# Kernel optimization log

Measured on AMD Instinct MI355X. Metric: run time of the kernel, lower is better.

Reference implementation:

```python
import jax, jax.numpy as jnp
import numpy as np

BQ = 64  # query block size
BK = 64  # key block size
PV_SCALE = 1e-3  # pvthreshd (~0..50) -> prob threshold, mirrors int8 P-quantization cutoff


def setup_inputs() -> dict:
    key = jax.random.key(0)
    ks = jax.random.split(key, 6)
    B, H, L, D = 2, 16, 2048, 64
    q = jax.random.normal(ks[0], (B, H, L, D), jnp.float32)
    k = jax.random.normal(ks[1], (B, H, L, D), jnp.float32)
    v = jax.random.normal(ks[2], (B, H, L, D), jnp.float32)
    # per-head tuned thresholds (init defaults / autotune ranges)
    cdfthreshd = 0.85 + 0.14 * jax.random.uniform(ks[3], (H,), jnp.float32)
    simthreshd1 = jax.random.uniform(ks[4], (H,), jnp.float32, minval=-0.3, maxval=0.5)
    pvthreshd = jax.random.uniform(ks[5], (H,), jnp.float32, minval=15.0, maxval=25.0)
    return dict(q=q, k=k, v=v, cdfthreshd=cdfthreshd,
                simthreshd1=simthreshd1, pvthreshd=pvthreshd)


def _sparse_meansim_attention(q, k, v, cdfthreshd, simthreshd1, pvthreshd):
    B, H, L, D = q.shape
    nqb, nkb = L // BQ, L // BK
    scale = 1.0 / jnp.sqrt(jnp.float32(D))

    # smooth_k: subtract per-(B,H) key mean along sequence
    k = k - k.mean(axis=2, keepdims=True)

    qb = q.reshape(B, H, nqb, BQ, D)
    kb = k.reshape(B, H, nkb, BK, D)
    qm = qb.mean(axis=3)  # [B,H,nqb,D]
    km = kb.mean(axis=3)  # [B,H,nkb,D]

    # mean cosine similarity of queries to their block mean -> pooled (prunable) blocks
    qn = jnp.linalg.norm(qb, axis=-1)            # [B,H,nqb,BQ]
    qmn = jnp.linalg.norm(qm, axis=-1)           # [B,H,nqb]
    cos = jnp.einsum('bhnqd,bhnd->bhnq', qb, qm) / (qn * qmn[..., None] + 1e-6)
    pooled = cos.mean(axis=-1) > simthreshd1[None, :, None]  # [B,H,nqb]

    # block-level score map from pooled means, CDF-based top-mass block selection
    s = jnp.einsum('bhid,bhjd->bhij', qm, km) * scale        # [B,H,nqb,nkb]
    p = jax.nn.softmax(s, axis=-1)
    order = jnp.argsort(-p, axis=-1)
    p_sorted = jnp.take_along_axis(p, order, axis=-1)
    excl_cdf = jnp.cumsum(p_sorted, axis=-1) - p_sorted      # exclusive CDF
    keep_sorted = excl_cdf < cdfthreshd[None, :, None, None]
    keep = jnp.take_along_axis(keep_sorted, jnp.argsort(order, axis=-1), axis=-1)

    sink = (jnp.arange(nkb) == 0)  # attention_sink: always keep first key block
    block_mask = keep | (~pooled)[..., None] | sink          # [B,H,nqb,nkb]

    # full attention restricted to selected blocks
    S = jnp.einsum('bhqd,bhkd->bhqk', q, k) * scale          # [B,H,L,L]
    m = jnp.repeat(jnp.repeat(block_mask, BQ, axis=2), BK, axis=3)
    P = jax.nn.softmax(jnp.where(m, S, -jnp.inf), axis=-1)

    # second-stage PV pruning: skip PV accumulation for negligible prob blocks
    Pb = P.reshape(B, H, nqb, BQ, nkb, BK)
    pv_keep = Pb.max(axis=(3, 5)) >= pvthreshd[None, :, None, None] * PV_SCALE
    pv_keep = pv_keep | sink
    Pb = Pb * pv_keep[:, :, :, None, :, None].astype(P.dtype)

    o = jnp.einsum('bhqk,bhkd->bhqd', Pb.reshape(B, H, L, L), v)
    return o


def reference(q, k, v, cdfthreshd, simthreshd1, pvthreshd):
    return _sparse_meansim_attention(q, k, v, cdfthreshd, simthreshd1, pvthreshd)
```

## Files before the change

### kernel.cpp

```cpp
#include <hip/hip_runtime.h>
#include <hip/hip_bf16.h>
#include <math.h>
#include <stdint.h>

#define B 2
#define H 16
#define L 2048
#define D 64
#define NB 32
#define PTS 72

typedef unsigned short u16;
typedef unsigned int u32;
typedef __attribute__((ext_vector_type(2))) unsigned int u32x2;
typedef __attribute__((ext_vector_type(4))) unsigned int u32x4;
typedef __attribute__((ext_vector_type(8))) short s16x8;
typedef __attribute__((ext_vector_type(4))) float f32x4;

union FragU { s16x8 v; u32 u[4]; };

__device__ __forceinline__ u32 pkbf(float a, float b) {
  __hip_bfloat162 h = __float22bfloat162_rn(make_float2(a, b));
  union { __hip_bfloat162 h; u32 u; } cv; cv.h = h; return cv.u;
}
__device__ __forceinline__ float bf2f(u32 u16bits) {
  union { u32 u; float f; } c; c.u = u16bits << 16; return c.f;
}
__device__ __forceinline__ void split4(float4 p, u32x2& hi, u32x2& lo) {
  u32 h01 = pkbf(p.x, p.y), h23 = pkbf(p.z, p.w);
  float rx = p.x - bf2f(h01 & 0xffffu);
  float ry = p.y - bf2f(h01 >> 16);
  float rz = p.z - bf2f(h23 & 0xffffu);
  float rw = p.w - bf2f(h23 >> 16);
  hi = (u32x2){h01, h23};
  lo = (u32x2){pkbf(rx, ry), pkbf(rz, rw)};
}

__global__ __launch_bounds__(256) void k_prep(const float* __restrict__ k,
                                              const float* __restrict__ v,
                                              float* __restrict__ ksum,
                                              u16* __restrict__ khi_g,
                                              u16* __restrict__ klo_g,
                                              u16* __restrict__ vthi_g,
                                              u16* __restrict__ vtlo_g,
                                              float* __restrict__ kbmax) {
  int blk = blockIdx.x, bh = blk >> 5, j = blk & 31, t = threadIdx.x;
  int lane = t & 63, w = t >> 6;
  __shared__ float vt[64 * 65];
  __shared__ float pk_[4][64];
  __shared__ unsigned bmaxS;
  if (t == 0) bmaxS = 0u;
  size_t base = (size_t)blk * 4096;

  int r0 = t >> 3;
  int c8 = (t & 7) * 8;
  float cs[8] = {0.f, 0.f, 0.f, 0.f, 0.f, 0.f, 0.f, 0.f};
  float rmax = 0.f;
#pragma unroll
  for (int it = 0; it < 2; ++it) {
    int r = r0 + 32 * it;
    const float* kp = k + base + r * 64 + c8;
    float4 f0 = *(const float4*)kp;
    float4 f1 = *(const float4*)(kp + 4);
    u32x2 h0, l0, h1, l1;
    split4(f0, h0, l0); split4(f1, h1, l1);
    *(u32x4*)(khi_g + base + r * 64 + c8) = (u32x4){h0[0], h0[1], h1[0], h1[1]};
    *(u32x4*)(klo_g + base + r * 64 + c8) = (u32x4){l0[0], l0[1], l1[0], l1[1]};
    cs[0] += f0.x; cs[1] += f0.y; cs[2] += f0.z; cs[3] += f0.w;
    cs[4] += f1.x; cs[5] += f1.y; cs[6] += f1.z; cs[7] += f1.w;
    float ssq = f0.x*f0.x + f0.y*f0.y + f0.z*f0.z + f0.w*f0.w
              + f1.x*f1.x + f1.y*f1.y + f1.z*f1.z + f1.w*f1.w;
    ssq += __shfl_xor(ssq, 1); ssq += __shfl_xor(ssq, 2); ssq += __shfl_xor(ssq, 4);
    if ((t & 7) == 0) rmax = fmaxf(rmax, ssq);
    const float* vp = v + base + r * 64 + c8;
    float4 g0 = *(const float4*)vp;
    float4 g1 = *(const float4*)(vp + 4);
    vt[(c8 + 0) * 65 + r] = g0.x;
    vt[(c8 + 1) * 65 + r] = g0.y;
    vt[(c8 + 2) * 65 + r] = g0.z;
    vt[(c8 + 3) * 65 + r] = g0.w;
    vt[(c8 + 4) * 65 + r] = g1.x;
    vt[(c8 + 5) * 65 + r] = g1.y;
    vt[(c8 + 6) * 65 + r] = g1.z;
    vt[(c8 + 7) * 65 + r] = g1.w;
  }
  if ((t & 7) == 0) atomicMax(&bmaxS, __float_as_uint(rmax));
#pragma unroll
  for (int i = 0; i < 8; ++i) {
    cs[i] += __shfl_xor(cs[i], 8);
    cs[i] += __shfl_xor(cs[i], 16);
    cs[i] += __shfl_xor(cs[i], 32);
  }
  if (lane < 8) {
    *(float4*)&pk_[w][lane * 8]     = (float4){cs[0], cs[1], cs[2], cs[3]};
    *(float4*)&pk_[w][lane * 8 + 4] = (float4){cs[4], cs[5], cs[6], cs[7]};
  }
  __syncthreads();
  if (t < 64) ksum[(size_t)blk * 64 + t] = pk_[0][t] + pk_[1][t] + pk_[2][t] + pk_[3][t];
  if (t == 0) kbmax[blk] = __uint_as_float(bmaxS);
#pragma unroll
  for (int it = 0; it < 2; ++it) {
    int idx = t + 256 * it, d = idx >> 3, s8 = (idx & 7) * 8;
    const float* vr = &vt[d * 65 + s8];
    float4 f0 = {vr[0], vr[1], vr[2], vr[3]};
    float4 f1 = {vr[4], vr[5], vr[6], vr[7]};
    u32x2 h0, l0, h1, l1;
    split4(f0, h0, l0); split4(f1, h1, l1);
    size_t o = (size_t)bh * 131072 + (size_t)d * 2048 + j * 64 + s8;
    *(u32x4*)(vthi_g + o) = (u32x4){h0[0], h0[1], h1[0], h1[1]};
    *(u32x4*)(vtlo_g + o) = (u32x4){l0[0], l0[1], l1[0], l1[1]};
  }
}

#define RBM_OFF 36864
#define MS_OFF 53760
#define LINV_OFF 54272
#define LPART_OFF 54784
#define QM_OFF 56832
#define FLG_OFF 57344

__global__ __launch_bounds__(256, 2) void k_attn(
    const float* __restrict__ q,
    const float* __restrict__ ksum,
    const u16* __restrict__ khi_g, const u16* __restrict__ klo_g,
    const u16* __restrict__ vthi_g, const u16* __restrict__ vtlo_g,
    const float* __restrict__ cdfthreshd, const float* __restrict__ simthreshd1,
    const float* __restrict__ pvthreshd, const float* __restrict__ kbmax,
    float* __restrict__ out) {
  int blk0 = blockIdx.x;
  int blk = (blk0 & 7) * 64 + (blk0 >> 3);
  int bh = blk >> 4, ip = blk & 15, h = bh & (H - 1);
  int t = threadIdx.x, lane = t & 63, w = t >> 6;
  int m16 = lane & 15, quad = lane >> 4;

  __shared__ __align__(16) uint8_t smem[57376];
  u16*   pbase = (u16*)smem;
  u32*   rbm0  = (u32*)(smem + RBM_OFF);
  float* MS    = (float*)(smem + MS_OFF);
  float* linvS = (float*)(smem + LINV_OFF);
  float* lpart = (float*)(smem + LPART_OFF);
  float* qmS   = (float*)(smem + QM_OFF);
  int*   flg   = (int*)(smem + FLG_OFF);
#define PHQ(qb) (pbase + (qb) * 9216)
#define PLQ(qb) (pbase + 4608 + (qb) * 9216)

  const float* qg0 = q + ((size_t)bh * L + (size_t)(2 * ip) * 64) * D;
  const float* qg1 = qg0 + 64 * D;
  const u16* kh = khi_g + (size_t)bh * (L * D);
  const u16* kl = klo_g + (size_t)bh * (L * D);
  const u16* vh = vthi_g + (size_t)bh * (L * D);
  const u16* vl = vtlo_g + (size_t)bh * (L * D);

  s16x8 qhf[2][4][2], qlf[2][4][2];
#pragma unroll
  for (int qb = 0; qb < 2; ++qb) {
    const float* qgq = qb ? qg1 : qg0;
#pragma unroll
    for (int nt = 0; nt < 4; ++nt)
#pragma unroll
      for (int ks = 0; ks < 2; ++ks) {
        const float* p0 = qgq + (16 * nt + m16) * 64 + ks * 32 + quad * 8;
        float4 a = *(const float4*)p0;
        float4 b2 = *(const float4*)(p0 + 4);
        u32x2 ha, la, hb, lb;
        split4(a, ha, la); split4(b2, hb, lb);
        FragU fh, fl;
        fh.u[0] = ha[0]; fh.u[1] = ha[1]; fh.u[2] = hb[0]; fh.u[3] = hb[1];
        fl.u[0] = la[0]; fl.u[1] = la[1]; fl.u[2] = lb[0]; fl.u[3] = lb[1];
        qhf[qb][nt][ks] = fh.v; qlf[qb][nt][ks] = fl.v;
      }
  }
  for (int e = t; e < 2 * 64 * 33; e += 256)
    rbm0[e] = 0x7F800000u;

  if (w == 0 || w == 2) {
    int qb = w >> 1;
    const float* qgq = qb ? qg1 : qg0;
    float s = 0.f;
    for (int r = 0; r < 64; ++r) s += qgq[r * 64 + lane];
    qmS[qb * 64 + lane] = s * (1.f / 64.f);
  }
  if (w == 1) {
    float m = (lane < 32) ? kbmax[bh * 32 + lane] : 0.f;
    for (int off = 16; off; off >>= 1) m = fmaxf(m, __shfl_xor(m, off, 32));
    if (lane == 0) ((float*)flg)[6] = m;
  }
  __syncthreads();

  bool keepj = false;
  if ((w == 0 || w == 2) && lane < 32) {
    int qb = w >> 1, j = lane;
    const float* qmv = qmS + qb * 64;
    const float* ksp = ksum + (size_t)bh * NB * 64 + j * 64;
    float sv = 0.f;
    for (int d = 0; d < 64; ++d) sv += qmv[d] * ksp[d];
    sv *= (1.f / 64.f) * 0.125f;
    float mx = sv;
    for (int off = 16; off; off >>= 1) mx = fmaxf(mx, __shfl_xor(mx, off, 32));
    float p = expf(sv - mx);
    float sum = p;
    for (int off = 16; off; off >>= 1) sum += __shfl_xor(sum, off, 32);
    p /= sum;
    float excl = 0.f;
    for (int u = 0; u < 32; ++u) {
      float pu = __shfl(p, u, 32);
      if ((pu > p) || (pu == p && u < j)) excl += pu;
    }
    keepj = excl < cdfthreshd[h];
  }
  if (w == 1 || w == 3) {
    int qb = w >> 1, r = lane;
    const float* qgq = qb ? qg1 : qg0;
    const float* qmv = qmS + qb * 64;
    float kmax2 = ((float*)flg)[6];
    float dot = 0.f, qn2 = 0.f, qmn2 = 0.f;
    for (int d = 0; d < 64; ++d) {
      float a = qgq[r * 64 + d], b2 = qmv[d];
      dot += a * b2; qn2 += a * a; qmn2 += b2 * b2;
    }
    float cs = dot / (sqrtf(qn2) * sqrtf(qmn2) + 1e-6f);
    float su = cs;
    for (int off = 32; off; off >>= 1) su += __shfl_xor(su, off);
    if (lane == 0) flg[qb] = (su * (1.f / 64.f)) > simthreshd1[h];
    MS[qb * 64 + r] = sqrtf(qn2 * kmax2) * 0.125f;
  }
  __syncthreads();
  if ((w == 0 || w == 2) && lane < 32) {
    int qb = w >> 1;
    bool bit = keepj || !flg[qb] || (lane == 0);
    unsigned long long bal = __ballot(bit);
    if (lane == 0) flg[2 + qb] = (int)(u32)bal;
  }
  __syncthreads();
  u32 mw0 = (u32)flg[2], mw1 = (u32)flg[3];

  float Mq[2][4];
#pragma unroll
  for (int qb = 0; qb < 2; ++qb)
#pragma unroll
    for (int nt = 0; nt < 4; ++nt) Mq[qb][nt] = MS[qb * 64 + 16 * nt + m16];

  float lp[2][4] = {{0.f,0.f,0.f,0.f},{0.f,0.f,0.f,0.f}};
  {
    u32 mwU = mw0 | mw1;
    int j = (int)__builtin_ctz(mwU);
    u32 rm_ = mwU & (mwU - 1);
    s16x8 ka[2][2], kan[2][2];
    {
      const u16* kr0 = kh + (size_t)(j * 64 + 16 * w + m16) * 64 + quad * 8;
      const u16* kl0 = kl + (size_t)(j * 64 + 16 * w + m16) * 64 + quad * 8;
#pragma unroll
      for (int ks = 0; ks < 2; ++ks) {
        ka[ks][0] = *(const s16x8*)(kr0 + ks * 32);
        ka[ks][1] = *(const s16x8*)(kl0 + ks * 32);
      }
    }
    for (;;) {
      int nj = -1;
      if (rm_) {
        nj = (int)__builtin_ctz(rm_); rm_ &= rm_ - 1;
        const u16* nr = kh + (size_t)(nj * 64 + 16 * w + m16) * 64 + quad * 8;
        const u16* nl = kl + (size_t)(nj * 64 + 16 * w + m16) * 64 + quad * 8;
#pragma unroll
        for (int ks = 0; ks < 2; ++ks) {
          kan[ks][0] = *(const s16x8*)(nr + ks * 32);
          kan[ks][1] = *(const s16x8*)(nl + ks * 32);
        }
      }
#pragma unroll
      for (int qb = 0; qb < 2; ++qb) {
        u32 mm = qb ? mw1 : mw0;
        if (!((mm >> j) & 1u)) continue;
        f32x4 acc[4];
#pragma unroll
        for (int nt = 0; nt < 4; ++nt) acc[nt] = (f32x4){0.f, 0.f, 0.f, 0.f};
#pragma unroll
        for (int ks = 0; ks < 2; ++ks)
#pragma unroll
          for (int nt = 0; nt < 4; ++nt) {
            acc[nt] = __builtin_amdgcn_mfma_f32_16x16x32_bf16(ka[ks][0], qhf[qb][nt][ks], acc[nt], 0, 0, 0);
            acc[nt] = __builtin_amdgcn_mfma_f32_16x16x32_bf16(ka[ks][1], qhf[qb][nt][ks], acc[nt], 0, 0, 0);
            acc[nt] = __builtin_amdgcn_mfma_f32_16x16x32_bf16(ka[ks][0], qlf[qb][nt][ks], acc[nt], 0, 0, 0);
          }
#pragma unroll
        for (int nt = 0; nt < 4; ++nt) {
          float vmax = -1e30f;
#pragma unroll
          for (int reg = 0; reg < 4; ++reg) {
            float s = acc[nt][reg] * 0.125f - Mq[qb][nt];
            lp[qb][nt] += __expf(s);
            vmax = fmaxf(vmax, s);
          }
          vmax = fmaxf(vmax, __shfl_xor(vmax, 16));
          vmax = fmaxf(vmax, __shfl_xor(vmax, 32));
          if (quad == 0)
            atomicMin(rbm0 + qb * (64 * 33) + (16 * nt + m16) * 33 + j,
                      __float_as_uint(fmaxf(-vmax, 0.f)));
        }
      }
      if (nj < 0) break;
#pragma unroll
      for (int ks = 0; ks < 2; ++ks) { ka[ks][0] = kan[ks][0]; ka[ks][1] = kan[ks][1]; }
      j = nj;
    }
  }
#pragma unroll
  for (int qb = 0; qb < 2; ++qb)
#pragma unroll
    for (int nt = 0; nt < 4; ++nt) {
      float s = lp[qb][nt];
      s += __shfl_xor(s, 16); s += __shfl_xor(s, 32);
      if (quad == 0) lpart[w * 128 + qb * 64 + 16 * nt + m16] = s;
    }
  __syncthreads();
  if (t < 128) linvS[t] = 1.f / (lpart[t] + lpart[128 + t] + lpart[256 + t] + lpart[384 + t]);
  __syncthreads();

  if (w < 2 && lane < 32) {
    u32 mm = w ? mw1 : mw0;
    bool keep = (mm >> lane) & 1u;
    if (keep && lane != 0) {
      float thr = pvthreshd[h] * 1e-3f;
      const float* lin = linvS + w * 64;
      const u32* rb = rbm0 + w * (64 * 33);
      float mp = 0.f;
      for (int r = 0; r < 64; ++r) {
        float key = __uint_as_float(rb[r * 33 + lane]);
        mp = fmaxf(mp, __expf(-key) * lin[r]);
      }
      keep = mp >= thr;
    }
    unsigned long long bal = __ballot(keep);
    if (lane == 0) flg[4 + w] = (int)(u32)bal;
  }
  __syncthreads();
  u32 gm0 = (u32)flg[4], gm1 = (u32)flg[5];

  float linq[2][4];
#pragma unroll
  for (int qb = 0; qb < 2; ++qb)
#pragma unroll
    for (int nt = 0; nt < 4; ++nt) linq[qb][nt] = linvS[qb * 64 + 16 * nt + m16];
  f32x4 oacc[2][4];
#pragma unroll
  for (int qb = 0; qb < 2; ++qb)
#pragma unroll
    for (int nt = 0; nt < 4; ++nt) oacc[qb][nt] = (f32x4){0.f, 0.f, 0.f, 0.f};

  {
    u32 gmU = gm0 | gm1;
    int j = -1;
    u32 g2 = gmU;
    s16x8 ka[2][2];
    if (g2) {
      j = (int)__builtin_ctz(g2); g2 &= g2 - 1;
      const u16* kr0 = kh + (size_t)(j * 64 + 16 * w + m16) * 64 + quad * 8;
      const u16* kl0 = kl + (size_t)(j * 64 + 16 * w + m16) * 64 + quad * 8;
#pragma unroll
      for (int ks = 0; ks < 2; ++ks) {
        ka[ks][0] = *(const s16x8*)(kr0 + ks * 32);
        ka[ks][1] = *(const s16x8*)(kl0 + ks * 32);
      }
    }
    while (j >= 0) {
      int in0 = (gm0 >> j) & 1, in1 = (gm1 >> j) & 1;
      s16x8 va[2][2];
      {
        const u16* vr0 = vh + (size_t)(16 * w + m16) * L + j * 64 + quad * 8;
        const u16* vl0 = vl + (size_t)(16 * w + m16) * L + j * 64 + quad * 8;
#pragma unroll
        for (int ks = 0; ks < 2; ++ks) {
          va[ks][0] = *(const s16x8*)(vr0 + ks * 32);
          va[ks][1] = *(const s16x8*)(vl0 + ks * 32);
        }
      }
      f32x4 acc[4];
      if (in0) {
#pragma unroll
        for (int nt = 0; nt < 4; ++nt) acc[nt] = (f32x4){0.f, 0.f, 0.f, 0.f};
#pragma unroll
        for (int ks = 0; ks < 2; ++ks)
#pragma unroll
          for (int nt = 0; nt < 4; ++nt) {
            acc[nt] = __builtin_amdgcn_mfma_f32_16x16x32_bf16(ka[ks][0], qhf[0][nt][ks], acc[nt], 0, 0, 0);
            acc[nt] = __builtin_amdgcn_mfma_f32_16x16x32_bf16(ka[ks][1], qhf[0][nt][ks], acc[nt], 0, 0, 0);
            acc[nt] = __builtin_amdgcn_mfma_f32_16x16x32_bf16(ka[ks][0], qlf[0][nt][ks], acc[nt], 0, 0, 0);
          }
      }
      __syncthreads();
      if (in0) {
#pragma unroll
        for (int nt = 0; nt < 4; ++nt) {
          float4 pv;
          pv.x = __expf(acc[nt][0] * 0.125f - Mq[0][nt]) * linq[0][nt];
          pv.y = __expf(acc[nt][1] * 0.125f - Mq[0][nt]) * linq[0][nt];
          pv.z = __expf(acc[nt][2] * 0.125f - Mq[0][nt]) * linq[0][nt];
          pv.w = __expf(acc[nt][3] * 0.125f - Mq[0][nt]) * linq[0][nt];
          u32x2 hi, lo; split4(pv, hi, lo);
          int off = (16 * nt + m16) * PTS + 16 * w + 4 * quad;
          *(u32x2*)(PHQ(0) + off) = hi;
          *(u32x2*)(PLQ(0) + off) = lo;
        }
      }
      if (in1) {
#pragma unroll
        for (int nt = 0; nt < 4; ++nt) acc[nt] = (f32x4){0.f, 0.f, 0.f, 0.f};
#pragma unroll
        for (int ks = 0; ks < 2; ++ks)
#pragma unroll
          for (int nt = 0; nt < 4; ++nt) {
            acc[nt] = __builtin_amdgcn_mfma_f32_16x16x32_bf16(ka[ks][0], qhf[1][nt][ks], acc[nt], 0, 0, 0);
            acc[nt] = __builtin_amdgcn_mfma_f32_16x16x32_bf16(ka[ks][1], qhf[1][nt][ks], acc[nt], 0, 0, 0);
            acc[nt] = __builtin_amdgcn_mfma_f32_16x16x32_bf16(ka[ks][0], qlf[1][nt][ks], acc[nt], 0, 0, 0);
          }
#pragma unroll
        for (int nt = 0; nt < 4; ++nt) {
          float4 pv;
          pv.x = __expf(acc[nt][0] * 0.125f - Mq[1][nt]) * linq[1][nt];
          pv.y = __expf(acc[nt][1] * 0.125f - Mq[1][nt]) * linq[1][nt];
          pv.z = __expf(acc[nt][2] * 0.125f - Mq[1][nt]) * linq[1][nt];
          pv.w = __expf(acc[nt][3] * 0.125f - Mq[1][nt]) * linq[1][nt];
          u32x2 hi, lo; split4(pv, hi, lo);
          int off = (16 * nt + m16) * PTS + 16 * w + 4 * quad;
          *(u32x2*)(PHQ(1) + off) = hi;
          *(u32x2*)(PLQ(1) + off) = lo;
        }
      }
      int nj = -1;
      if (g2) {
        nj = (int)__builtin_ctz(g2); g2 &= g2 - 1;
        const u16* nr = kh + (size_t)(nj * 64 + 16 * w + m16) * 64 + quad * 8;
        const u16* nl = kl + (size_t)(nj * 64 + 16 * w + m16) * 64 + quad * 8;
#pragma unroll
        for (int ks = 0; ks < 2; ++ks) {
          ka[ks][0] = *(const s16x8*)(nr + ks * 32);
          ka[ks][1] = *(const s16x8*)(nl + ks * 32);
        }
      }
      __syncthreads();
#pragma unroll
      for (int qb = 0; qb < 2; ++qb) {
        if (!(qb ? in1 : in0)) continue;
        const u16* ph_ = PHQ(qb);
        const u16* pl_ = PLQ(qb);
#pragma unroll
        for (int ks = 0; ks < 2; ++ks)
#pragma unroll
          for (int nt = 0; nt < 4; ++nt) {
            s16x8 pbh = *(const s16x8*)(ph_ + (16 * nt + m16) * PTS + ks * 32 + quad * 8);
            s16x8 pbl = *(const s16x8*)(pl_ + (16 * nt + m16) * PTS + ks * 32 + quad * 8);
            oacc[qb][nt] = __builtin_amdgcn_mfma_f32_16x16x32_bf16(va[ks][0], pbh, oacc[qb][nt], 0, 0, 0);
            oacc[qb][nt] = __builtin_amdgcn_mfma_f32_16x16x32_bf16(va[ks][1], pbh, oacc[qb][nt], 0, 0, 0);
            oacc[qb][nt] = __builtin_amdgcn_mfma_f32_16x16x32_bf16(va[ks][0], pbl, oacc[qb][nt], 0, 0, 0);
          }
      }
      j = nj;
    }
  }

#pragma unroll
  for (int qb = 0; qb < 2; ++qb) {
    float* ob = out + ((size_t)bh * L + (size_t)(2 * ip + qb) * 64) * D;
#pragma unroll
    for (int nt = 0; nt < 4; ++nt)
      *(f32x4*)(ob + (16 * nt + m16) * 64 + 16 * w + 4 * quad) = oacc[qb][nt];
  }
}

extern "C" void kernel_launch(void* const* d_in, const int* in_sizes, int n_in,
                              void* d_out, int out_size, void* d_ws, size_t ws_size,
                              hipStream_t stream) {
  (void)in_sizes; (void)n_in; (void)out_size; (void)ws_size;
  const float* q   = (const float*)d_in[0];
  const float* k   = (const float*)d_in[1];
  const float* v   = (const float*)d_in[2];
  const float* cdf = (const float*)d_in[3];
  const float* sim = (const float*)d_in[4];
  const float* pvt = (const float*)d_in[5];
  float* out = (float*)d_out;

  uint8_t* w8 = (uint8_t*)d_ws;
  float* ksum  = (float*)w8;
  float* kbmax = (float*)(w8 + 262144);
  u16* khi_g  = (u16*)(w8 + 266240);
  u16* klo_g  = khi_g + (size_t)B * H * L * D;
  u16* vthi_g = klo_g + (size_t)B * H * L * D;
  u16* vtlo_g = vthi_g + (size_t)B * H * L * D;

  k_prep<<<B * H * NB, 256, 0, stream>>>(k, v, ksum, khi_g, klo_g, vthi_g, vtlo_g, kbmax);
  k_attn<<<B * H * NB / 2, 256, 0, stream>>>(q, ksum, khi_g, klo_g, vthi_g, vtlo_g,
                                             cdf, sim, pvt, kbmax, out);
}
```

Measured before the change: 211.9 us.

## Process one query block per workgroup with per-wave query rows

```diff
diff --git a/kernel.cpp b/kernel.cpp
--- a/kernel.cpp
+++ b/kernel.cpp
@@ -112,14 +112,7 @@
   }
 }
 
-#define RBM_OFF 36864
-#define MS_OFF 53760
-#define LINV_OFF 54272
-#define LPART_OFF 54784
-#define QM_OFF 56832
-#define FLG_OFF 57344
-
-__global__ __launch_bounds__(256, 2) void k_attn(
+__global__ __launch_bounds__(256, 4) void k_attn(
     const float* __restrict__ q,
     const float* __restrict__ ksum,
     const u16* __restrict__ khi_g, const u16* __restrict__ klo_g,
@@ -128,72 +121,58 @@
     const float* __restrict__ pvthreshd, const float* __restrict__ kbmax,
     float* __restrict__ out) {
   int blk0 = blockIdx.x;
-  int blk = (blk0 & 7) * 64 + (blk0 >> 3);
-  int bh = blk >> 4, ip = blk & 15, h = bh & (H - 1);
+  int blk = (blk0 & 7) * 128 + (blk0 >> 3);
+  int bh = blk >> 5, iq = blk & 31, h = bh & (H - 1);
   int t = threadIdx.x, lane = t & 63, w = t >> 6;
   int m16 = lane & 15, quad = lane >> 4;
 
-  __shared__ __align__(16) uint8_t smem[57376];
+  __shared__ __align__(16) uint8_t smem[27680];
   u16*   pbase = (u16*)smem;
-  u32*   rbm0  = (u32*)(smem + RBM_OFF);
-  float* MS    = (float*)(smem + MS_OFF);
-  float* linvS = (float*)(smem + LINV_OFF);
-  float* lpart = (float*)(smem + LPART_OFF);
-  float* qmS   = (float*)(smem + QM_OFF);
-  int*   flg   = (int*)(smem + FLG_OFF);
-#define PHQ(qb) (pbase + (qb) * 9216)
-#define PLQ(qb) (pbase + 4608 + (qb) * 9216)
-
-  const float* qg0 = q + ((size_t)bh * L + (size_t)(2 * ip) * 64) * D;
-  const float* qg1 = qg0 + 64 * D;
+  float* rbm   = (float*)(smem + 18432);
+  float* MSs   = (float*)(smem + 26880);
+  float* linvS = (float*)(smem + 27136);
+  float* qmS   = (float*)(smem + 27392);
+  int*   flg   = (int*)(smem + 27648);
+
+  const float* qg = q + ((size_t)bh * L + (size_t)iq * 64) * D;
   const u16* kh = khi_g + (size_t)bh * (L * D);
   const u16* kl = klo_g + (size_t)bh * (L * D);
   const u16* vh = vthi_g + (size_t)bh * (L * D);
   const u16* vl = vtlo_g + (size_t)bh * (L * D);
 
-  s16x8 qhf[2][4][2], qlf[2][4][2];
-#pragma unroll
-  for (int qb = 0; qb < 2; ++qb) {
-    const float* qgq = qb ? qg1 : qg0;
-#pragma unroll
-    for (int nt = 0; nt < 4; ++nt)
-#pragma unroll
-      for (int ks = 0; ks < 2; ++ks) {
-        const float* p0 = qgq + (16 * nt + m16) * 64 + ks * 32 + quad * 8;
-        float4 a = *(const float4*)p0;
-        float4 b2 = *(const float4*)(p0 + 4);
-        u32x2 ha, la, hb, lb;
-        split4(a, ha, la); split4(b2, hb, lb);
-        FragU fh, fl;
-        fh.u[0] = ha[0]; fh.u[1] = ha[1]; fh.u[2] = hb[0]; fh.u[3] = hb[1];
-        fl.u[0] = la[0]; fl.u[1] = la[1]; fl.u[2] = lb[0]; fl.u[3] = lb[1];
-        qhf[qb][nt][ks] = fh.v; qlf[qb][nt][ks] = fl.v;
-      }
-  }
-  for (int e = t; e < 2 * 64 * 33; e += 256)
-    rbm0[e] = 0x7F800000u;
-
-  if (w == 0 || w == 2) {
-    int qb = w >> 1;
-    const float* qgq = qb ? qg1 : qg0;
+  s16x8 qh[2], ql[2];
+#pragma unroll
+  for (int ks = 0; ks < 2; ++ks) {
+    const float* p0 = qg + (size_t)(16 * w + m16) * 64 + ks * 32 + quad * 8;
+    float4 a = *(const float4*)p0;
+    float4 b2 = *(const float4*)(p0 + 4);
+    u32x2 ha, la, hb, lb;
+    split4(a, ha, la); split4(b2, hb, lb);
+    FragU fh, fl;
+    fh.u[0] = ha[0]; fh.u[1] = ha[1]; fh.u[2] = hb[0]; fh.u[3] = hb[1];
+    fl.u[0] = la[0]; fl.u[1] = la[1]; fl.u[2] = lb[0]; fl.u[3] = lb[1];
+    qh[ks] = fh.v; ql[ks] = fl.v;
+  }
+  for (int e = t; e < 64 * 33; e += 256) rbm[e] = __builtin_inff();
+
+  if (w == 0) {
     float s = 0.f;
-    for (int r = 0; r < 64; ++r) s += qgq[r * 64 + lane];
-    qmS[qb * 64 + lane] = s * (1.f / 64.f);
+    for (int r = 0; r < 64; ++r) s += qg[r * 64 + lane];
+    qmS[lane] = s * (1.f / 64.f);
   }
   if (w == 1) {
     float m = (lane < 32) ? kbmax[bh * 32 + lane] : 0.f;
     for (int off = 16; off; off >>= 1) m = fmaxf(m, __shfl_xor(m, off, 32));
-    if (lane == 0) ((float*)flg)[6] = m;
+    if (lane == 0) ((float*)flg)[3] = m;
   }
   __syncthreads();
 
   bool keepj = false;
-  if ((w == 0 || w == 2) && lane < 32) {
-    int qb = w >> 1, j = lane;
-    const float* qmv = qmS + qb * 64;
+  if (w == 0 && lane < 32) {
+    int j = lane;
     const float* ksp = ksum + (size_t)bh * NB * 64 + j * 64;
     float sv = 0.f;
-    for (int d = 0; d < 64; ++d) sv += qmv[d] * ksp[d];
+    for (int d = 0; d < 64; ++d) sv += qmS[d] * ksp[d];
     sv *= (1.f / 64.f) * 0.125f;
     float mx = sv;
     for (int off = 16; off; off >>= 1) mx = fmaxf(mx, __shfl_xor(mx, off, 32));
@@ -208,263 +187,197 @@
     }
     keepj = excl < cdfthreshd[h];
   }
-  if (w == 1 || w == 3) {
-    int qb = w >> 1, r = lane;
-    const float* qgq = qb ? qg1 : qg0;
-    const float* qmv = qmS + qb * 64;
-    float kmax2 = ((float*)flg)[6];
+  if (w == 1) {
+    int r = lane;
+    float kmax2 = ((float*)flg)[3];
     float dot = 0.f, qn2 = 0.f, qmn2 = 0.f;
     for (int d = 0; d < 64; ++d) {
-      float a = qgq[r * 64 + d], b2 = qmv[d];
+      float a = qg[r * 64 + d], b2 = qmS[d];
       dot += a * b2; qn2 += a * a; qmn2 += b2 * b2;
     }
     float cs = dot / (sqrtf(qn2) * sqrtf(qmn2) + 1e-6f);
     float su = cs;
     for (int off = 32; off; off >>= 1) su += __shfl_xor(su, off);
-    if (lane == 0) flg[qb] = (su * (1.f / 64.f)) > simthreshd1[h];
-    MS[qb * 64 + r] = sqrtf(qn2 * kmax2) * 0.125f;
-  }
-  __syncthreads();
-  if ((w == 0 || w == 2) && lane < 32) {
-    int qb = w >> 1;
-    bool bit = keepj || !flg[qb] || (lane == 0);
+    if (lane == 0) flg[0] = (su * (1.f / 64.f)) > simthreshd1[h];
+    MSs[r] = sqrtf(qn2 * kmax2) * 0.125f;
+  }
+  __syncthreads();
+  if (w == 0 && lane < 32) {
+    bool bit = keepj || !flg[0] || (lane == 0);
     unsigned long long bal = __ballot(bit);
-    if (lane == 0) flg[2 + qb] = (int)(u32)bal;
-  }
-  __syncthreads();
-  u32 mw0 = (u32)flg[2], mw1 = (u32)flg[3];
-
-  float Mq[2][4];
-#pragma unroll
-  for (int qb = 0; qb < 2; ++qb)
-#pragma unroll
-    for (int nt = 0; nt < 4; ++nt) Mq[qb][nt] = MS[qb * 64 + 16 * nt + m16];
-
-  float lp[2][4] = {{0.f,0.f,0.f,0.f},{0.f,0.f,0.f,0.f}};
+    if (lane == 0) flg[1] = (int)(u32)bal;
+  }
+  __syncthreads();
+  u32 mw = (u32)flg[1];
+
+  float Mq[4];
+#pragma unroll
+  for (int reg = 0; reg < 4; ++reg) Mq[reg] = MSs[16 * w + 4 * quad + reg];
+
+  float lp[4] = {0.f, 0.f, 0.f, 0.f};
   {
-    u32 mwU = mw0 | mw1;
-    int j = (int)__builtin_ctz(mwU);
-    u32 rm_ = mwU & (mwU - 1);
-    s16x8 ka[2][2], kan[2][2];
-    {
-      const u16* kr0 = kh + (size_t)(j * 64 + 16 * w + m16) * 64 + quad * 8;
-      const u16* kl0 = kl + (size_t)(j * 64 + 16 * w + m16) * 64 + quad * 8;
-#pragma unroll
-      for (int ks = 0; ks < 2; ++ks) {
-        ka[ks][0] = *(const s16x8*)(kr0 + ks * 32);
-        ka[ks][1] = *(const s16x8*)(kl0 + ks * 32);
+    u32 rm = mw;
+    while (rm) {
+      int j = (int)__builtin_ctz(rm); rm &= rm - 1;
+      const u16* kbh_ = kh + (size_t)(j * 64) * 64;
+      const u16* kbl_ = kl + (size_t)(j * 64) * 64;
+      float vmx[4] = {-1e30f, -1e30f, -1e30f, -1e30f};
+#pragma unroll
+      for (int half = 0; half < 2; ++half) {
+        s16x8 kfh[2][2], kfl[2][2];
+#pragma unroll
+        for (int ktp = 0; ktp < 2; ++ktp) {
+          const u16* rh = kbh_ + (size_t)(16 * (2 * half + ktp) + m16) * 64 + quad * 8;
+          const u16* rl = kbl_ + (size_t)(16 * (2 * half + ktp) + m16) * 64 + quad * 8;
+#pragma unroll
+          for (int ks = 0; ks < 2; ++ks) {
+            kfh[ktp][ks] = *(const s16x8*)(rh + ks * 32);
+            kfl[ktp][ks] = *(const s16x8*)(rl + ks * 32);
+          }
+        }
+        f32x4 acc[2] = {{0.f,0.f,0.f,0.f},{0.f,0.f,0.f,0.f}};
+        __builtin_amdgcn_s_setprio(1);
+#pragma unroll
+        for (int ks = 0; ks < 2; ++ks)
+#pragma unroll
+          for (int ktp = 0; ktp < 2; ++ktp) {
+            acc[ktp] = __builtin_amdgcn_mfma_f32_16x16x32_bf16(qh[ks], kfh[ktp][ks], acc[ktp], 0, 0, 0);
+            acc[ktp] = __builtin_amdgcn_mfma_f32_16x16x32_bf16(qh[ks], kfl[ktp][ks], acc[ktp], 0, 0, 0);
+            acc[ktp] = __builtin_amdgcn_mfma_f32_16x16x32_bf16(ql[ks], kfh[ktp][ks], acc[ktp], 0, 0, 0);
+          }
+        __builtin_amdgcn_s_setprio(0);
+#pragma unroll
+        for (int ktp = 0; ktp < 2; ++ktp)
+#pragma unroll
+          for (int reg = 0; reg < 4; ++reg) {
+            float s = acc[ktp][reg] * 0.125f - Mq[reg];
+            lp[reg] += __expf(s);
+            vmx[reg] = fmaxf(vmx[reg], s);
+          }
+      }
+#pragma unroll
+      for (int reg = 0; reg < 4; ++reg) {
+        float v = vmx[reg];
+        v = fmaxf(v, __shfl_xor(v, 1));
+        v = fmaxf(v, __shfl_xor(v, 2));
+        v = fmaxf(v, __shfl_xor(v, 4));
+        v = fmaxf(v, __shfl_xor(v, 8));
+        if (m16 == 0) rbm[(16 * w + 4 * quad + reg) * 33 + j] = fmaxf(-v, 0.f);
       }
     }
-    for (;;) {
-      int nj = -1;
-      if (rm_) {
-        nj = (int)__builtin_ctz(rm_); rm_ &= rm_ - 1;
-        const u16* nr = kh + (size_t)(nj * 64 + 16 * w + m16) * 64 + quad * 8;
-        const u16* nl = kl + (size_t)(nj * 64 + 16 * w + m16) * 64 + quad * 8;
-#pragma unroll
-        for (int ks = 0; ks < 2; ++ks) {
-          kan[ks][0] = *(const s16x8*)(nr + ks * 32);
-          kan[ks][1] = *(const s16x8*)(nl + ks * 32);
-        }
-      }
-#pragma unroll
-      for (int qb = 0; qb < 2; ++qb) {
-        u32 mm = qb ? mw1 : mw0;
-        if (!((mm >> j) & 1u)) continue;
-        f32x4 acc[4];
-#pragma unroll
-        for (int nt = 0; nt < 4; ++nt) acc[nt] = (f32x4){0.f, 0.f, 0.f, 0.f};
-#pragma unroll
-        for (int ks = 0; ks < 2; ++ks)
-#pragma unroll
-          for (int nt = 0; nt < 4; ++nt) {
-            acc[nt] = __builtin_amdgcn_mfma_f32_16x16x32_bf16(ka[ks][0], qhf[qb][nt][ks], acc[nt], 0, 0, 0);
-            acc[nt] = __builtin_amdgcn_mfma_f32_16x16x32_bf16(ka[ks][1], qhf[qb][nt][ks], acc[nt], 0, 0, 0);
-            acc[nt] = __builtin_amdgcn_mfma_f32_16x16x32_bf16(ka[ks][0], qlf[qb][nt][ks], acc[nt], 0, 0, 0);
-          }
-#pragma unroll
-        for (int nt = 0; nt < 4; ++nt) {
-          float vmax = -1e30f;
-#pragma unroll
-          for (int reg = 0; reg < 4; ++reg) {
-            float s = acc[nt][reg] * 0.125f - Mq[qb][nt];
-            lp[qb][nt] += __expf(s);
-            vmax = fmaxf(vmax, s);
-          }
-          vmax = fmaxf(vmax, __shfl_xor(vmax, 16));
-          vmax = fmaxf(vmax, __shfl_xor(vmax, 32));
-          if (quad == 0)
-            atomicMin(rbm0 + qb * (64 * 33) + (16 * nt + m16) * 33 + j,
-                      __float_as_uint(fmaxf(-vmax, 0.f)));
-        }
-      }
-      if (nj < 0) break;
-#pragma unroll
-      for (int ks = 0; ks < 2; ++ks) { ka[ks][0] = kan[ks][0]; ka[ks][1] = kan[ks][1]; }
-      j = nj;
-    }
-  }
-#pragma unroll
-  for (int qb = 0; qb < 2; ++qb)
-#pragma unroll
-    for (int nt = 0; nt < 4; ++nt) {
-      float s = lp[qb][nt];
-      s += __shfl_xor(s, 16); s += __shfl_xor(s, 32);
-      if (quad == 0) lpart[w * 128 + qb * 64 + 16 * nt + m16] = s;
-    }
-  __syncthreads();
-  if (t < 128) linvS[t] = 1.f / (lpart[t] + lpart[128 + t] + lpart[256 + t] + lpart[384 + t]);
-  __syncthreads();
-
-  if (w < 2 && lane < 32) {
-    u32 mm = w ? mw1 : mw0;
-    bool keep = (mm >> lane) & 1u;
+  }
+  float linq[4];
+#pragma unroll
+  for (int reg = 0; reg < 4; ++reg) {
+    float s = lp[reg];
+    s += __shfl_xor(s, 1); s += __shfl_xor(s, 2);
+    s += __shfl_xor(s, 4); s += __shfl_xor(s, 8);
+    linq[reg] = 1.f / s;
+    if (m16 == 0) linvS[16 * w + 4 * quad + reg] = linq[reg];
+  }
+  __syncthreads();
+
+  if (w == 0 && lane < 32) {
+    bool keep = (mw >> lane) & 1u;
     if (keep && lane != 0) {
       float thr = pvthreshd[h] * 1e-3f;
-      const float* lin = linvS + w * 64;
-      const u32* rb = rbm0 + w * (64 * 33);
       float mp = 0.f;
       for (int r = 0; r < 64; ++r) {
-        float key = __uint_as_float(rb[r * 33 + lane]);
-        mp = fmaxf(mp, __expf(-key) * lin[r]);
+        float key = rbm[r * 33 + lane];
+        mp = fmaxf(mp, __expf(-key) * linvS[r]);
       }
       keep = mp >= thr;
     }
     unsigned long long bal = __ballot(keep);
-    if (lane == 0) flg[4 + w] = (int)(u32)bal;
-  }
-  __syncthreads();
-  u32 gm0 = (u32)flg[4], gm1 = (u32)flg[5];
-
-  float linq[2][4];
-#pragma unroll
-  for (int qb = 0; qb < 2; ++qb)
-#pragma unroll
-    for (int nt = 0; nt < 4; ++nt) linq[qb][nt] = linvS[qb * 64 + 16 * nt + m16];
-  f32x4 oacc[2][4];
-#pragma unroll
-  for (int qb = 0; qb < 2; ++qb)
-#pragma unroll
-    for (int nt = 0; nt < 4; ++nt) oacc[qb][nt] = (f32x4){0.f, 0.f, 0.f, 0.f};
-
+    if (lane == 0) flg[2] = (int)(u32)bal;
+  }
+  __syncthreads();
+  u32 gm = (u32)flg[2];
+
+  f32x4 oacc[4];
+#pragma unroll
+  for (int dt = 0; dt < 4; ++dt) oacc[dt] = (f32x4){0.f, 0.f, 0.f, 0.f};
+  u16* phw = pbase + w * 2304;
+  u16* plw = phw + 1152;
   {
-    u32 gmU = gm0 | gm1;
-    int j = -1;
-    u32 g2 = gmU;
-    s16x8 ka[2][2];
-    if (g2) {
-      j = (int)__builtin_ctz(g2); g2 &= g2 - 1;
-      const u16* kr0 = kh + (size_t)(j * 64 + 16 * w + m16) * 64 + quad * 8;
-      const u16* kl0 = kl + (size_t)(j * 64 + 16 * w + m16) * 64 + quad * 8;
+    u32 rg = gm;
+    while (rg) {
+      int j = (int)__builtin_ctz(rg); rg &= rg - 1;
+      const u16* kbh_ = kh + (size_t)(j * 64) * 64;
+      const u16* kbl_ = kl + (size_t)(j * 64) * 64;
+#pragma unroll
+      for (int half = 0; half < 2; ++half) {
+        s16x8 kfh[2][2], kfl[2][2];
+#pragma unroll
+        for (int ktp = 0; ktp < 2; ++ktp) {
+          const u16* rh = kbh_ + (size_t)(16 * (2 * half + ktp) + m16) * 64 + quad * 8;
+          const u16* rl = kbl_ + (size_t)(16 * (2 * half + ktp) + m16) * 64 + quad * 8;
+#pragma unroll
+          for (int ks = 0; ks < 2; ++ks) {
+            kfh[ktp][ks] = *(const s16x8*)(rh + ks * 32);
+            kfl[ktp][ks] = *(const s16x8*)(rl + ks * 32);
+          }
+        }
+        f32x4 acc[2] = {{0.f,0.f,0.f,0.f},{0.f,0.f,0.f,0.f}};
+        __builtin_amdgcn_s_setprio(1);
+#pragma unroll
+        for (int ks = 0; ks < 2; ++ks)
+#pragma unroll
+          for (int ktp = 0; ktp < 2; ++ktp) {
+            acc[ktp] = __builtin_amdgcn_mfma_f32_16x16x32_bf16(qh[ks], kfh[ktp][ks], acc[ktp], 0, 0, 0);
+            acc[ktp] = __builtin_amdgcn_mfma_f32_16x16x32_bf16(qh[ks], kfl[ktp][ks], acc[ktp], 0, 0, 0);
+            acc[ktp] = __builtin_amdgcn_mfma_f32_16x16x32_bf16(ql[ks], kfh[ktp][ks], acc[ktp], 0, 0, 0);
+          }
+        __builtin_amdgcn_s_setprio(0);
+#pragma unroll
+        for (int ktp = 0; ktp < 2; ++ktp) {
+          int kt = 2 * half + ktp;
+#pragma unroll
+          for (int reg = 0; reg < 4; ++reg) {
+            float p = __expf(acc[ktp][reg] * 0.125f - Mq[reg]) * linq[reg];
+            union { __hip_bfloat16 b; u16 u; } ch, cl;
+            ch.b = __float2bfloat16(p);
+            cl.b = __float2bfloat16(p - bf2f(ch.u));
+            int off = (4 * quad + reg) * PTS + 16 * kt + m16;
+            phw[off] = ch.u;
+            plw[off] = cl.u;
+          }
+        }
+      }
+      s16x8 pbh[2], pbl[2];
 #pragma unroll
       for (int ks = 0; ks < 2; ++ks) {
-        ka[ks][0] = *(const s16x8*)(kr0 + ks * 32);
-        ka[ks][1] = *(const s16x8*)(kl0 + ks * 32);
+        pbh[ks] = *(const s16x8*)(phw + m16 * PTS + ks * 32 + quad * 8);
+        pbl[ks] = *(const s16x8*)(plw + m16 * PTS + ks * 32 + quad * 8);
+      }
+      const u16* vbh_ = vh + (size_t)j * 64;
+      const u16* vbl_ = vl + (size_t)j * 64;
+#pragma unroll
+      for (int dt = 0; dt < 4; ++dt) {
+        s16x8 vah[2], val_[2];
+        const u16* rh = vbh_ + (size_t)(16 * dt + m16) * L + quad * 8;
+        const u16* rl = vbl_ + (size_t)(16 * dt + m16) * L + quad * 8;
+#pragma unroll
+        for (int ks = 0; ks < 2; ++ks) {
+          vah[ks] = *(const s16x8*)(rh + ks * 32);
+          val_[ks] = *(const s16x8*)(rl + ks * 32);
+        }
+        __builtin_amdgcn_s_setprio(1);
+#pragma unroll
+        for (int ks = 0; ks < 2; ++ks) {
+          oacc[dt] = __builtin_amdgcn_mfma_f32_16x16x32_bf16(vah[ks], pbh[ks], oacc[dt], 0, 0, 0);
+          oacc[dt] = __builtin_amdgcn_mfma_f32_16x16x32_bf16(val_[ks], pbh[ks], oacc[dt], 0, 0, 0);
+          oacc[dt] = __builtin_amdgcn_mfma_f32_16x16x32_bf16(vah[ks], pbl[ks], oacc[dt], 0, 0, 0);
+        }
+        __builtin_amdgcn_s_setprio(0);
       }
     }
-    while (j >= 0) {
-      int in0 = (gm0 >> j) & 1, in1 = (gm1 >> j) & 1;
-      s16x8 va[2][2];
-      {
-        const u16* vr0 = vh + (size_t)(16 * w + m16) * L + j * 64 + quad * 8;
-        const u16* vl0 = vl + (size_t)(16 * w + m16) * L + j * 64 + quad * 8;
-#pragma unroll
-        for (int ks = 0; ks < 2; ++ks) {
-          va[ks][0] = *(const s16x8*)(vr0 + ks * 32);
-          va[ks][1] = *(const s16x8*)(vl0 + ks * 32);
-        }
-      }
-      f32x4 acc[4];
-      if (in0) {
-#pragma unroll
-        for (int nt = 0; nt < 4; ++nt) acc[nt] = (f32x4){0.f, 0.f, 0.f, 0.f};
-#pragma unroll
-        for (int ks = 0; ks < 2; ++ks)
-#pragma unroll
-          for (int nt = 0; nt < 4; ++nt) {
-            acc[nt] = __builtin_amdgcn_mfma_f32_16x16x32_bf16(ka[ks][0], qhf[0][nt][ks], acc[nt], 0, 0, 0);
-            acc[nt] = __builtin_amdgcn_mfma_f32_16x16x32_bf16(ka[ks][1], qhf[0][nt][ks], acc[nt], 0, 0, 0);
-            acc[nt] = __builtin_amdgcn_mfma_f32_16x16x32_bf16(ka[ks][0], qlf[0][nt][ks], acc[nt], 0, 0, 0);
-          }
-      }
-      __syncthreads();
-      if (in0) {
-#pragma unroll
-        for (int nt = 0; nt < 4; ++nt) {
-          float4 pv;
-          pv.x = __expf(acc[nt][0] * 0.125f - Mq[0][nt]) * linq[0][nt];
-          pv.y = __expf(acc[nt][1] * 0.125f - Mq[0][nt]) * linq[0][nt];
-          pv.z = __expf(acc[nt][2] * 0.125f - Mq[0][nt]) * linq[0][nt];
-          pv.w = __expf(acc[nt][3] * 0.125f - Mq[0][nt]) * linq[0][nt];
-          u32x2 hi, lo; split4(pv, hi, lo);
-          int off = (16 * nt + m16) * PTS + 16 * w + 4 * quad;
-          *(u32x2*)(PHQ(0) + off) = hi;
-          *(u32x2*)(PLQ(0) + off) = lo;
-        }
-      }
-      if (in1) {
-#pragma unroll
-        for (int nt = 0; nt < 4; ++nt) acc[nt] = (f32x4){0.f, 0.f, 0.f, 0.f};
-#pragma unroll
-        for (int ks = 0; ks < 2; ++ks)
-#pragma unroll
-          for (int nt = 0; nt < 4; ++nt) {
-            acc[nt] = __builtin_amdgcn_mfma_f32_16x16x32_bf16(ka[ks][0], qhf[1][nt][ks], acc[nt], 0, 0, 0);
-            acc[nt] = __builtin_amdgcn_mfma_f32_16x16x32_bf16(ka[ks][1], qhf[1][nt][ks], acc[nt], 0, 0, 0);
-            acc[nt] = __builtin_amdgcn_mfma_f32_16x16x32_bf16(ka[ks][0], qlf[1][nt][ks], acc[nt], 0, 0, 0);
-          }
-#pragma unroll
-        for (int nt = 0; nt < 4; ++nt) {
-          float4 pv;
-          pv.x = __expf(acc[nt][0] * 0.125f - Mq[1][nt]) * linq[1][nt];
-          pv.y = __expf(acc[nt][1] * 0.125f - Mq[1][nt]) * linq[1][nt];
-          pv.z = __expf(acc[nt][2] * 0.125f - Mq[1][nt]) * linq[1][nt];
-          pv.w = __expf(acc[nt][3] * 0.125f - Mq[1][nt]) * linq[1][nt];
-          u32x2 hi, lo; split4(pv, hi, lo);
-          int off = (16 * nt + m16) * PTS + 16 * w + 4 * quad;
-          *(u32x2*)(PHQ(1) + off) = hi;
-          *(u32x2*)(PLQ(1) + off) = lo;
-        }
-      }
-      int nj = -1;
-      if (g2) {
-        nj = (int)__builtin_ctz(g2); g2 &= g2 - 1;
-        const u16* nr = kh + (size_t)(nj * 64 + 16 * w + m16) * 64 + quad * 8;
-        const u16* nl = kl + (size_t)(nj * 64 + 16 * w + m16) * 64 + quad * 8;
-#pragma unroll
-        for (int ks = 0; ks < 2; ++ks) {
-          ka[ks][0] = *(const s16x8*)(nr + ks * 32);
-          ka[ks][1] = *(const s16x8*)(nl + ks * 32);
-        }
-      }
-      __syncthreads();
-#pragma unroll
-      for (int qb = 0; qb < 2; ++qb) {
-        if (!(qb ? in1 : in0)) continue;
-        const u16* ph_ = PHQ(qb);
-        const u16* pl_ = PLQ(qb);
-#pragma unroll
-        for (int ks = 0; ks < 2; ++ks)
-#pragma unroll
-          for (int nt = 0; nt < 4; ++nt) {
-            s16x8 pbh = *(const s16x8*)(ph_ + (16 * nt + m16) * PTS + ks * 32 + quad * 8);
-            s16x8 pbl = *(const s16x8*)(pl_ + (16 * nt + m16) * PTS + ks * 32 + quad * 8);
-            oacc[qb][nt] = __builtin_amdgcn_mfma_f32_16x16x32_bf16(va[ks][0], pbh, oacc[qb][nt], 0, 0, 0);
-            oacc[qb][nt] = __builtin_amdgcn_mfma_f32_16x16x32_bf16(va[ks][1], pbh, oacc[qb][nt], 0, 0, 0);
-            oacc[qb][nt] = __builtin_amdgcn_mfma_f32_16x16x32_bf16(va[ks][0], pbl, oacc[qb][nt], 0, 0, 0);
-          }
-      }
-      j = nj;
-    }
-  }
-
-#pragma unroll
-  for (int qb = 0; qb < 2; ++qb) {
-    float* ob = out + ((size_t)bh * L + (size_t)(2 * ip + qb) * 64) * D;
-#pragma unroll
-    for (int nt = 0; nt < 4; ++nt)
-      *(f32x4*)(ob + (16 * nt + m16) * 64 + 16 * w + 4 * quad) = oacc[qb][nt];
-  }
+  }
+
+  float* ob = out + ((size_t)bh * L + (size_t)iq * 64) * D;
+#pragma unroll
+  for (int dt = 0; dt < 4; ++dt)
+    *(f32x4*)(ob + (size_t)(16 * w + m16) * 64 + 16 * dt + 4 * quad) = oacc[dt];
 }
 
 extern "C" void kernel_launch(void* const* d_in, const int* in_sizes, int n_in,
@@ -488,6 +401,6 @@
   u16* vtlo_g = vthi_g + (size_t)B * H * L * D;
 
   k_prep<<<B * H * NB, 256, 0, stream>>>(k, v, ksum, khi_g, klo_g, vthi_g, vtlo_g, kbmax);
-  k_attn<<<B * H * NB / 2, 256, 0, stream>>>(q, ksum, khi_g, klo_g, vthi_g, vtlo_g,
-                                             cdf, sim, pvt, kbmax, out);
-}
+  k_attn<<<B * H * NB, 256, 0, stream>>>(q, ksum, khi_g, klo_g, vthi_g, vtlo_g,
+                                         cdf, sim, pvt, kbmax, out);
+}
```

New measurement: 427.1 us. +101.6%, slower.

## Shrink and swizzle shared P tiles, add MFMA priority, raise occupancy

Applied to the files above, without the earlier changes.

```diff
diff --git a/kernel.cpp b/kernel.cpp
--- a/kernel.cpp
+++ b/kernel.cpp
@@ -8,7 +8,6 @@
 #define L 2048
 #define D 64
 #define NB 32
-#define PTS 72
 
 typedef unsigned short u16;
 typedef unsigned int u32;
@@ -34,6 +33,9 @@
   float rw = p.w - bf2f(h23 >> 16);
   hi = (u32x2){h01, h23};
   lo = (u32x2){pkbf(rx, ry), pkbf(rz, rw)};
+}
+__device__ __forceinline__ int swz(int row, int colb) {
+  return (row << 7) + (colb ^ ((row & 7) << 4));
 }
 
 __global__ __launch_bounds__(256) void k_prep(const float* __restrict__ k,
@@ -112,14 +114,7 @@
   }
 }
 
-#define RBM_OFF 36864
-#define MS_OFF 53760
-#define LINV_OFF 54272
-#define LPART_OFF 54784
-#define QM_OFF 56832
-#define FLG_OFF 57344
-
-__global__ __launch_bounds__(256, 2) void k_attn(
+__global__ __launch_bounds__(256, 3) void k_attn(
     const float* __restrict__ q,
     const float* __restrict__ ksum,
     const u16* __restrict__ khi_g, const u16* __restrict__ klo_g,
@@ -133,16 +128,15 @@
   int t = threadIdx.x, lane = t & 63, w = t >> 6;
   int m16 = lane & 15, quad = lane >> 4;
 
-  __shared__ __align__(16) uint8_t smem[57376];
-  u16*   pbase = (u16*)smem;
-  u32*   rbm0  = (u32*)(smem + RBM_OFF);
-  float* MS    = (float*)(smem + MS_OFF);
-  float* linvS = (float*)(smem + LINV_OFF);
-  float* lpart = (float*)(smem + LPART_OFF);
-  float* qmS   = (float*)(smem + QM_OFF);
-  int*   flg   = (int*)(smem + FLG_OFF);
-#define PHQ(qb) (pbase + (qb) * 9216)
-#define PLQ(qb) (pbase + 4608 + (qb) * 9216)
+  __shared__ __align__(16) uint8_t smem[32800];
+  u32*   rbm0  = (u32*)smem;
+  float* lpart = (float*)(smem + 16896);
+  float* qmS   = (float*)(smem + 18944);
+  float* MSs   = (float*)(smem + 19456);
+  float* linvS = (float*)(smem + 19968);
+  int*   flg   = (int*)(smem + 32768);
+#define PHB(qb) (smem + (qb) * 16384)
+#define PLB(qb) (smem + (qb) * 16384 + 8192)
 
   const float* qg0 = q + ((size_t)bh * L + (size_t)(2 * ip) * 64) * D;
   const float* qg1 = qg0 + 64 * D;
@@ -222,7 +216,7 @@
     float su = cs;
     for (int off = 32; off; off >>= 1) su += __shfl_xor(su, off);
     if (lane == 0) flg[qb] = (su * (1.f / 64.f)) > simthreshd1[h];
-    MS[qb * 64 + r] = sqrtf(qn2 * kmax2) * 0.125f;
+    MSs[qb * 64 + r] = sqrtf(qn2 * kmax2) * 0.125f;
   }
   __syncthreads();
   if ((w == 0 || w == 2) && lane < 32) {
@@ -238,7 +232,7 @@
 #pragma unroll
   for (int qb = 0; qb < 2; ++qb)
 #pragma unroll
-    for (int nt = 0; nt < 4; ++nt) Mq[qb][nt] = MS[qb * 64 + 16 * nt + m16];
+    for (int nt = 0; nt < 4; ++nt) Mq[qb][nt] = MSs[qb * 64 + 16 * nt + m16];
 
   float lp[2][4] = {{0.f,0.f,0.f,0.f},{0.f,0.f,0.f,0.f}};
   {
@@ -274,6 +268,7 @@
         f32x4 acc[4];
 #pragma unroll
         for (int nt = 0; nt < 4; ++nt) acc[nt] = (f32x4){0.f, 0.f, 0.f, 0.f};
+        __builtin_amdgcn_s_setprio(1);
 #pragma unroll
         for (int ks = 0; ks < 2; ++ks)
 #pragma unroll
@@ -282,6 +277,7 @@
             acc[nt] = __builtin_amdgcn_mfma_f32_16x16x32_bf16(ka[ks][1], qhf[qb][nt][ks], acc[nt], 0, 0, 0);
             acc[nt] = __builtin_amdgcn_mfma_f32_16x16x32_bf16(ka[ks][0], qlf[qb][nt][ks], acc[nt], 0, 0, 0);
           }
+        __builtin_amdgcn_s_setprio(0);
 #pragma unroll
         for (int nt = 0; nt < 4; ++nt) {
           float vmax = -1e30f;
@@ -378,6 +374,7 @@
       if (in0) {
 #pragma unroll
         for (int nt = 0; nt < 4; ++nt) acc[nt] = (f32x4){0.f, 0.f, 0.f, 0.f};
+        __builtin_amdgcn_s_setprio(1);
 #pragma unroll
         for (int ks = 0; ks < 2; ++ks)
 #pragma unroll
@@ -386,6 +383,7 @@
             acc[nt] = __builtin_amdgcn_mfma_f32_16x16x32_bf16(ka[ks][1], qhf[0][nt][ks], acc[nt], 0, 0, 0);
             acc[nt] = __builtin_amdgcn_mfma_f32_16x16x32_bf16(ka[ks][0], qlf[0][nt][ks], acc[nt], 0, 0, 0);
           }
+        __builtin_amdgcn_s_setprio(0);
       }
       __syncthreads();
       if (in0) {
@@ -397,14 +395,15 @@
           pv.z = __expf(acc[nt][2] * 0.125f - Mq[0][nt]) * linq[0][nt];
           pv.w = __expf(acc[nt][3] * 0.125f - Mq[0][nt]) * linq[0][nt];
           u32x2 hi, lo; split4(pv, hi, lo);
-          int off = (16 * nt + m16) * PTS + 16 * w + 4 * quad;
-          *(u32x2*)(PHQ(0) + off) = hi;
-          *(u32x2*)(PLQ(0) + off) = lo;
+          int off = swz(16 * nt + m16, 32 * w + 8 * quad);
+          *(u32x2*)(PHB(0) + off) = hi;
+          *(u32x2*)(PLB(0) + off) = lo;
         }
       }
       if (in1) {
 #pragma unroll
         for (int nt = 0; nt < 4; ++nt) acc[nt] = (f32x4){0.f, 0.f, 0.f, 0.f};
+        __builtin_amdgcn_s_setprio(1);
 #pragma unroll
         for (int ks = 0; ks < 2; ++ks)
 #pragma unroll
@@ -413,6 +412,7 @@
             acc[nt] = __builtin_amdgcn_mfma_f32_16x16x32_bf16(ka[ks][1], qhf[1][nt][ks], acc[nt], 0, 0, 0);
             acc[nt] = __builtin_amdgcn_mfma_f32_16x16x32_bf16(ka[ks][0], qlf[1][nt][ks], acc[nt], 0, 0, 0);
           }
+        __builtin_amdgcn_s_setprio(0);
 #pragma unroll
         for (int nt = 0; nt < 4; ++nt) {
           float4 pv;
@@ -421,9 +421,9 @@
           pv.z = __expf(acc[nt][2] * 0.125f - Mq[1][nt]) * linq[1][nt];
           pv.w = __expf(acc[nt][3] * 0.125f - Mq[1][nt]) * linq[1][nt];
           u32x2 hi, lo; split4(pv, hi, lo);
-          int off = (16 * nt + m16) * PTS + 16 * w + 4 * quad;
-          *(u32x2*)(PHQ(1) + off) = hi;
-          *(u32x2*)(PLQ(1) + off) = lo;
+          int off = swz(16 * nt + m16, 32 * w + 8 * quad);
+          *(u32x2*)(PHB(1) + off) = hi;
+          *(u32x2*)(PLB(1) + off) = lo;
         }
       }
       int nj = -1;
@@ -441,17 +441,19 @@
 #pragma unroll
       for (int qb = 0; qb < 2; ++qb) {
         if (!(qb ? in1 : in0)) continue;
-        const u16* ph_ = PHQ(qb);
-        const u16* pl_ = PLQ(qb);
+        const uint8_t* ph_ = PHB(qb);
+        const uint8_t* pl_ = PLB(qb);
 #pragma unroll
         for (int ks = 0; ks < 2; ++ks)
 #pragma unroll
           for (int nt = 0; nt < 4; ++nt) {
-            s16x8 pbh = *(const s16x8*)(ph_ + (16 * nt + m16) * PTS + ks * 32 + quad * 8);
-            s16x8 pbl = *(const s16x8*)(pl_ + (16 * nt + m16) * PTS + ks * 32 + quad * 8);
+            s16x8 pbh = *(const s16x8*)(ph_ + swz(16 * nt + m16, ks * 64 + quad * 16));
+            s16x8 pbl = *(const s16x8*)(pl_ + swz(16 * nt + m16, ks * 64 + quad * 16));
+            __builtin_amdgcn_s_setprio(1);
             oacc[qb][nt] = __builtin_amdgcn_mfma_f32_16x16x32_bf16(va[ks][0], pbh, oacc[qb][nt], 0, 0, 0);
             oacc[qb][nt] = __builtin_amdgcn_mfma_f32_16x16x32_bf16(va[ks][1], pbh, oacc[qb][nt], 0, 0, 0);
             oacc[qb][nt] = __builtin_amdgcn_mfma_f32_16x16x32_bf16(va[ks][0], pbl, oacc[qb][nt], 0, 0, 0);
+            __builtin_amdgcn_s_setprio(0);
           }
       }
       j = nj;
```

Result: slower. 395.4 us (+86.6%).
